# Optimization experiments

Hardware: AMD Instinct MI355X
Metric: run time of the kernel (lower is better)

The kernel has to match this reference:

```python
import jax, jax.numpy as jnp
import numpy as np

NUM_HEADS = 16

def setup_inputs() -> dict:
    key = jax.random.key(0)
    k1, k2, k3 = jax.random.split(key, 3)
    B, N, C = 4, 2048, 1024
    x = jax.random.normal(k1, (B, N, C), dtype=jnp.float32)
    # torch Linear weights are [out_features, in_features]
    w_qkv = jax.random.normal(k2, (3 * C, C), dtype=jnp.float32) * (1.0 / np.sqrt(C))
    w_out = jax.random.normal(k3, (C, C), dtype=jnp.float32) * (1.0 / np.sqrt(C))
    b_out = jnp.zeros((C,), dtype=jnp.float32)
    return {"x": x, "w_qkv": w_qkv, "w_out": w_out, "b_out": b_out}

def reference(x, w_qkv, w_out, b_out):
    B, N, C = x.shape
    H = NUM_HEADS
    D = C // H
    scale = 1.0 / np.sqrt(D).astype(np.float32)
    # qkv projection: [B,N,3C] -> [3,B,H,N,D]
    qkv = (x @ w_qkv.T).reshape(B, N, 3, H, D).transpose(2, 0, 3, 1, 4)
    q, k, v = qkv[0], qkv[1], qkv[2]
    # The torch module's block-wise online softmax telescopes to exact softmax.
    scores = jnp.einsum("bhqd,bhkd->bhqk", q, k) * scale
    attn = jax.nn.softmax(scores, axis=-1)
    out = jnp.einsum("bhqk,bhkd->bhqd", attn, v)  # [B,H,N,D]
    out = out.transpose(0, 2, 1, 3).reshape(B, N, C)
    return out @ w_out.T + b_out
```

## Files before the change

### kernel.cpp

```cpp
#include <hip/hip_runtime.h>

typedef __attribute__((ext_vector_type(8))) short vbf8;
typedef __attribute__((ext_vector_type(4))) float vf4;

#define GLOAD16(g, l) __builtin_amdgcn_global_load_lds( \
    (const __attribute__((address_space(1))) void*)(g),  \
    (__attribute__((address_space(3))) void*)(l), 16, 0, 0)

__device__ __forceinline__ unsigned short f2bf(float f) {
  union { float f; unsigned u; } v; v.f = f;
  return (unsigned short)((v.u + 0x7fffu + ((v.u >> 16) & 1u)) >> 16);
}

__device__ __forceinline__ unsigned short cvt_bf16(float f) {
  __bf16 h = (__bf16)f;
  union { __bf16 h; unsigned short u; } v; v.h = h;
  return v.u;
}

__device__ __forceinline__ vf4 mfma16(vbf8 a, vbf8 b, vf4 c) {
  return __builtin_amdgcn_mfma_f32_16x16x32_bf16(a, b, c, 0, 0, 0);
}

__device__ __forceinline__ int swz(int row, int col) {
  return row * 64 + (col ^ ((row & 7) << 3));
}

__global__ __launch_bounds__(256)
void k_cvt_bf16(const float* __restrict__ in, unsigned short* __restrict__ out, int n4) {
  for (int i = blockIdx.x * blockDim.x + threadIdx.x; i < n4; i += gridDim.x * blockDim.x) {
    float4 v = ((const float4*)in)[i];
    ushort4 o;
    o.x = f2bf(v.x); o.y = f2bf(v.y); o.z = f2bf(v.z); o.w = f2bf(v.w);
    ((ushort4*)out)[i] = o;
  }
}

__global__ __launch_bounds__(256, 2)
void k_gemm_qkv(const unsigned short* __restrict__ A,
                const unsigned short* __restrict__ B,
                unsigned short* __restrict__ qb,
                unsigned short* __restrict__ kb,
                unsigned short* __restrict__ vb) {
  __shared__ unsigned short As[128 * 64];
  __shared__ unsigned short Bs[128 * 64];
  const int tid = threadIdx.x;
  const int lane = tid & 63;
  const int wid = tid >> 6;
  const int wm = wid >> 1, wn = wid & 1;
  const int flat = blockIdx.y * 24 + blockIdx.x;
  const int sw = (flat & 7) * 192 + (flat >> 3);
  const int m0 = (sw / 24) * 128;
  const int n0 = (sw % 24) * 128;
  const int l15 = lane & 15, kg = lane >> 4;
  const int srow = wid * 32 + (lane >> 3);
  const int scol = (lane & 7) * 8;

  vf4 acc[4][4] = {};

  for (int kt = 0; kt < 16; ++kt) {
    __syncthreads();
    const unsigned short* gA = A + (size_t)(m0 + srow) * 1024 + kt * 64 + scol;
    const unsigned short* gB = B + (size_t)(n0 + srow) * 1024 + kt * 64 + scol;
    const unsigned ab = (unsigned)(wid * 32 * 64);
#pragma unroll
    for (int i = 0; i < 4; ++i) {
      GLOAD16(gA + (size_t)i * 8 * 1024, &As[ab + i * 8 * 64]);
      GLOAD16(gB + (size_t)i * 8 * 1024, &Bs[ab + i * 8 * 64]);
    }
    __syncthreads();
#pragma unroll
    for (int kk = 0; kk < 2; ++kk) {
      vbf8 af[4], bfr[4];
#pragma unroll
      for (int mi = 0; mi < 4; ++mi)
        af[mi] = *(const vbf8*)&As[(wm * 64 + mi * 16 + l15) * 64 + kk * 32 + kg * 8];
#pragma unroll
      for (int ni = 0; ni < 4; ++ni)
        bfr[ni] = *(const vbf8*)&Bs[(wn * 64 + ni * 16 + l15) * 64 + kk * 32 + kg * 8];
#pragma unroll
      for (int mi = 0; mi < 4; ++mi)
#pragma unroll
        for (int ni = 0; ni < 4; ++ni)
          acc[mi][ni] = mfma16(af[mi], bfr[ni], acc[mi][ni]);
    }
  }

#pragma unroll
  for (int ni = 0; ni < 4; ++ni) {
    const int c = n0 + wn * 64 + ni * 16 + l15;
    const int which = c >> 10;
    const int hd = c & 1023;
    unsigned short* dst = (which == 0) ? qb : ((which == 1) ? kb : vb);
    const float sc = (which == 0) ? 0.18033688011112042f : 1.0f;
#pragma unroll
    for (int mi = 0; mi < 4; ++mi) {
#pragma unroll
      for (int r = 0; r < 4; ++r) {
        const int m = m0 + wm * 64 + mi * 16 + kg * 4 + r;
        const int b = m >> 11, nn = m & 2047;
        const size_t idx = (((size_t)(b * 16 + (hd >> 6)) * 2048 + nn) * 64) + (hd & 63);
        dst[idx] = f2bf(acc[mi][ni][r] * sc);
      }
    }
  }
}

__global__ __launch_bounds__(256)
void k_transpose_v(const unsigned short* __restrict__ vb, unsigned short* __restrict__ vt) {
  __shared__ unsigned short t[64][72];
  const int bh = blockIdx.y, n0 = blockIdx.x * 64;
  const int tid = threadIdx.x;
#pragma unroll
  for (int p = 0; p < 2; ++p) {
    const int r = p * 32 + (tid >> 3);
    vbf8 v = *(const vbf8*)&vb[((size_t)bh * 2048 + n0 + r) * 64 + (tid & 7) * 8];
    *(vbf8*)&t[r][(tid & 7) * 8] = v;
  }
  __syncthreads();
  const int d = tid >> 2, jb = (tid & 3) * 16;
  unsigned short buf[16];
#pragma unroll
  for (int j = 0; j < 16; ++j) buf[j] = t[jb + j][d];
  unsigned short* o = &vt[((size_t)bh * 64 + d) * 2048 + n0 + jb];
  *(vbf8*)&o[0] = *(vbf8*)&buf[0];
  *(vbf8*)&o[8] = *(vbf8*)&buf[8];
}

__global__ __launch_bounds__(256, 4)
void k_attn(const unsigned short* __restrict__ qb,
            const unsigned short* __restrict__ kb,
            const unsigned short* __restrict__ vt,
            unsigned short* __restrict__ ob) {
  __shared__ unsigned short Ks[2][64 * 64];
  __shared__ unsigned short Vs[64 * 64];
  __shared__ unsigned short Ps[4][32][64];
  const int tid = threadIdx.x, lane = tid & 63, w = tid >> 6;
  const int l15 = lane & 15, kg = lane >> 4;
  const int flat = blockIdx.x;
  const int sw = (flat & 7) * 128 + (flat >> 3);
  const int qt = sw & 15, bh = sw >> 4;

  const unsigned short* Q = qb + ((size_t)bh * 2048 + qt * 128 + w * 32) * 64;
  vbf8 qf[2][2];
#pragma unroll
  for (int qj = 0; qj < 2; ++qj)
#pragma unroll
    for (int kk = 0; kk < 2; ++kk)
      qf[qj][kk] = *(const vbf8*)(Q + (qj * 16 + l15) * 64 + kk * 32 + kg * 8);

  vbf8 onesv;
#pragma unroll
  for (int i = 0; i < 8; ++i) onesv[i] = (short)0x3F80;

  vf4 oacc[2][4] = {};
  vf4 lacc[2] = {};
  float mrun[2] = {-3.0e38f, -3.0e38f};

  const int srow = lane >> 3;
  const int scol = (((lane & 7) ^ srow) * 8);
  const int pswz = (l15 & 7) << 3;
  const unsigned short* gKbase = kb + ((size_t)bh * 2048 + w * 16 + srow) * 64 + scol;
  const unsigned short* gVbase = vt + ((size_t)bh * 64 + w * 16 + srow) * 2048 + scol;

#define STAGE_K(t, b) do { \
    const unsigned short* gK_ = gKbase + (size_t)(t) * 4096; \
    GLOAD16(gK_,       &Ks[b][(w * 16) * 64]); \
    GLOAD16(gK_ + 512, &Ks[b][(w * 16 + 8) * 64]); \
  } while (0)
#define STAGE_V(t) do { \
    const unsigned short* gV_ = gVbase + (size_t)(t) * 64; \
    GLOAD16(gV_,                 &Vs[(w * 16) * 64]); \
    GLOAD16(gV_ + (size_t)16384, &Vs[(w * 16 + 8) * 64]); \
  } while (0)

  STAGE_K(0, 0);
  asm volatile("s_waitcnt vmcnt(0)" ::: "memory");
  __builtin_amdgcn_s_barrier();
  __builtin_amdgcn_sched_barrier(0);

  for (int kt = 0; kt < 32; ++kt) {
    const int cur = kt & 1;
    STAGE_V(kt);
    if (kt + 1 < 32) STAGE_K(kt + 1, cur ^ 1);

    vf4 s[2][4] = {};
    __builtin_amdgcn_s_setprio(1);
#pragma unroll
    for (int kk = 0; kk < 2; ++kk)
#pragma unroll
      for (int ni = 0; ni < 4; ++ni) {
        const vbf8 kf = *(const vbf8*)&Ks[cur][swz(ni * 16 + l15, kk * 32 + kg * 8)];
        s[0][ni] = mfma16(kf, qf[0][kk], s[0][ni]);
        s[1][ni] = mfma16(kf, qf[1][kk], s[1][ni]);
      }
    __builtin_amdgcn_s_setprio(0);

#pragma unroll
    for (int qj = 0; qj < 2; ++qj) {
      float a0 = fmaxf(fmaxf(s[qj][0][0], s[qj][0][1]), fmaxf(s[qj][0][2], s[qj][0][3]));
      float a1 = fmaxf(fmaxf(s[qj][1][0], s[qj][1][1]), fmaxf(s[qj][1][2], s[qj][1][3]));
      float a2 = fmaxf(fmaxf(s[qj][2][0], s[qj][2][1]), fmaxf(s[qj][2][2], s[qj][2][3]));
      float a3 = fmaxf(fmaxf(s[qj][3][0], s[qj][3][1]), fmaxf(s[qj][3][2], s[qj][3][3]));
      float rm = fmaxf(fmaxf(a0, a1), fmaxf(a2, a3));
      rm = fmaxf(rm, __shfl_xor(rm, 16));
      rm = fmaxf(rm, __shfl_xor(rm, 32));

      if (__any(rm > mrun[qj] + 8.0f)) {
        const float mn = fmaxf(mrun[qj], rm);
        const float alpha = __builtin_amdgcn_exp2f(mrun[qj] - mn);
        mrun[qj] = mn;
        float av[4];
#pragma unroll
        for (int r = 0; r < 4; ++r) av[r] = __shfl(alpha, kg * 4 + r);
#pragma unroll
        for (int r = 0; r < 4; ++r) {
          lacc[qj][r] *= av[r];
#pragma unroll
          for (int ni = 0; ni < 4; ++ni) oacc[qj][ni][r] *= av[r];
        }
      }

#pragma unroll
      for (int ni = 0; ni < 4; ++ni) {
        ushort4 pk;
        pk.x = cvt_bf16(__builtin_amdgcn_exp2f(s[qj][ni][0] - mrun[qj]));
        pk.y = cvt_bf16(__builtin_amdgcn_exp2f(s[qj][ni][1] - mrun[qj]));
        pk.z = cvt_bf16(__builtin_amdgcn_exp2f(s[qj][ni][2] - mrun[qj]));
        pk.w = cvt_bf16(__builtin_amdgcn_exp2f(s[qj][ni][3] - mrun[qj]));
        *(ushort4*)&Ps[w][qj * 16 + l15][(ni * 16 + kg * 4) ^ pswz] = pk;
      }
    }

    if (kt + 1 < 32) asm volatile("s_waitcnt vmcnt(2) lgkmcnt(0)" ::: "memory");
    else             asm volatile("s_waitcnt vmcnt(0) lgkmcnt(0)" ::: "memory");
    __builtin_amdgcn_s_barrier();
    __builtin_amdgcn_sched_barrier(0);

    __builtin_amdgcn_s_setprio(1);
#pragma unroll
    for (int kk = 0; kk < 2; ++kk) {
      const vbf8 pf0 = *(const vbf8*)&Ps[w][l15][(kk * 32 + kg * 8) ^ pswz];
      const vbf8 pf1 = *(const vbf8*)&Ps[w][16 + l15][(kk * 32 + kg * 8) ^ pswz];
      lacc[0] = mfma16(pf0, onesv, lacc[0]);
      lacc[1] = mfma16(pf1, onesv, lacc[1]);
#pragma unroll
      for (int ni = 0; ni < 4; ++ni) {
        const vbf8 vf = *(const vbf8*)&Vs[swz(ni * 16 + l15, kk * 32 + kg * 8)];
        oacc[0][ni] = mfma16(pf0, vf, oacc[0][ni]);
        oacc[1][ni] = mfma16(pf1, vf, oacc[1][ni]);
      }
    }
    __builtin_amdgcn_s_setprio(0);

    __syncthreads();
  }
#undef STAGE_K
#undef STAGE_V

  const int b = bh >> 4, h = bh & 15;
#pragma unroll
  for (int qj = 0; qj < 2; ++qj)
#pragma unroll
    for (int r = 0; r < 4; ++r) {
      const float inv = 1.0f / lacc[qj][r];
      const int q = qt * 128 + w * 32 + qj * 16 + kg * 4 + r;
#pragma unroll
      for (int ni = 0; ni < 4; ++ni)
        ob[((size_t)b * 2048 + q) * 1024 + h * 64 + ni * 16 + l15] = cvt_bf16(oacc[qj][ni][r] * inv);
    }
}

__global__ __launch_bounds__(256, 2)
void k_gemm_out(const unsigned short* __restrict__ A,
                const unsigned short* __restrict__ B,
                const float* __restrict__ bias,
                float* __restrict__ out) {
  __shared__ unsigned short As[128 * 64];
  __shared__ unsigned short Bs[128 * 64];
  const int tid = threadIdx.x;
  const int lane = tid & 63;
  const int wid = tid >> 6;
  const int wm = wid >> 1, wn = wid & 1;
  const int flat = blockIdx.y * 8 + blockIdx.x;
  const int sw = (flat & 7) * 64 + (flat >> 3);
  const int m0 = (sw / 8) * 128;
  const int n0 = (sw % 8) * 128;
  const int l15 = lane & 15, kg = lane >> 4;
  const int srow = wid * 32 + (lane >> 3);
  const int scol = (lane & 7) * 8;

  vf4 acc[4][4] = {};

  for (int kt = 0; kt < 16; ++kt) {
    __syncthreads();
    const unsigned short* gA = A + (size_t)(m0 + srow) * 1024 + kt * 64 + scol;
    const unsigned short* gB = B + (size_t)(n0 + srow) * 1024 + kt * 64 + scol;
    const unsigned ab = (unsigned)(wid * 32 * 64);
#pragma unroll
    for (int i = 0; i < 4; ++i) {
      GLOAD16(gA + (size_t)i * 8 * 1024, &As[ab + i * 8 * 64]);
      GLOAD16(gB + (size_t)i * 8 * 1024, &Bs[ab + i * 8 * 64]);
    }
    __syncthreads();
#pragma unroll
    for (int kk = 0; kk < 2; ++kk) {
      vbf8 af[4], bfr[4];
#pragma unroll
      for (int mi = 0; mi < 4; ++mi)
        af[mi] = *(const vbf8*)&As[(wm * 64 + mi * 16 + l15) * 64 + kk * 32 + kg * 8];
#pragma unroll
      for (int ni = 0; ni < 4; ++ni)
        bfr[ni] = *(const vbf8*)&Bs[(wn * 64 + ni * 16 + l15) * 64 + kk * 32 + kg * 8];
#pragma unroll
      for (int mi = 0; mi < 4; ++mi)
#pragma unroll
        for (int ni = 0; ni < 4; ++ni)
          acc[mi][ni] = mfma16(af[mi], bfr[ni], acc[mi][ni]);
    }
  }

#pragma unroll
  for (int ni = 0; ni < 4; ++ni) {
    const int c = n0 + wn * 64 + ni * 16 + l15;
    const float bv = bias[c];
#pragma unroll
    for (int mi = 0; mi < 4; ++mi) {
#pragma unroll
      for (int r = 0; r < 4; ++r) {
        const int m = m0 + wm * 64 + mi * 16 + kg * 4 + r;
        out[(size_t)m * 1024 + c] = acc[mi][ni][r] + bv;
      }
    }
  }
}

extern "C" void kernel_launch(void* const* d_in, const int* in_sizes, int n_in,
                              void* d_out, int out_size, void* d_ws, size_t ws_size,
                              hipStream_t stream) {
  const float* x     = (const float*)d_in[0];
  const float* w_qkv = (const float*)d_in[1];
  const float* w_out = (const float*)d_in[2];
  const float* b_out = (const float*)d_in[3];
  float* out = (float*)d_out;

  char* ws = (char*)d_ws;
  unsigned short* xbf   = (unsigned short*)(ws);
  unsigned short* wqkvb = (unsigned short*)(ws + 16777216);
  unsigned short* woutb = (unsigned short*)(ws + 23068672);
  unsigned short* qbuf  = (unsigned short*)(ws + 25165824);
  unsigned short* kbuf  = (unsigned short*)(ws + 41943040);
  unsigned short* vbuf  = (unsigned short*)(ws + 58720256);
  unsigned short* vtbuf = (unsigned short*)(ws + 75497472);
  unsigned short* aob   = xbf;

  k_cvt_bf16<<<2048, 256, 0, stream>>>(x, xbf, 8388608 / 4);
  k_cvt_bf16<<<768, 256, 0, stream>>>(w_qkv, wqkvb, 3145728 / 4);
  k_cvt_bf16<<<256, 256, 0, stream>>>(w_out, woutb, 1048576 / 4);

  k_gemm_qkv<<<dim3(24, 64), 256, 0, stream>>>(xbf, wqkvb, qbuf, kbuf, vbuf);
  k_transpose_v<<<dim3(32, 64), 256, 0, stream>>>(vbuf, vtbuf);
  k_attn<<<dim3(1024), 256, 0, stream>>>(qbuf, kbuf, vtbuf, aob);
  k_gemm_out<<<dim3(8, 64), 256, 0, stream>>>(aob, woutb, b_out, out);
}
```

Measured before the change: 215.4 us.

## Double-buffer GEMMs with BK=32, fuse V transpose into QKV epilogue

Both GEMMs move from single-buffered BK=64 tiles with two barriers per step to double-buffered BK=32 tiles with XOR-swizzled LDS, prefetching the next tile while MFMAs run. The QKV GEMM becomes a 128x192 tile computed by 512 threads. Its epilogue writes V directly in transposed layout, which removes the separate transpose kernel and its round trip through memory. The attention row-max now uses a chain of three-input max operations. The transposed V stores are strided scalar writes, which may lower store efficiency in the epilogue.

```diff
diff --git a/kernel.cpp b/kernel.cpp
--- a/kernel.cpp
+++ b/kernel.cpp
@@ -20,6 +20,10 @@
 
 __device__ __forceinline__ vf4 mfma16(vbf8 a, vbf8 b, vf4 c) {
   return __builtin_amdgcn_mfma_f32_16x16x32_bf16(a, b, c, 0, 0, 0);
+}
+
+__device__ __forceinline__ float fmax3(float a, float b, float c) {
+  return fmaxf(fmaxf(a, b), c);
 }
 
 __device__ __forceinline__ int swz(int row, int col) {
@@ -36,62 +40,73 @@
   }
 }
 
-__global__ __launch_bounds__(256, 2)
+__global__ __launch_bounds__(512, 4)
 void k_gemm_qkv(const unsigned short* __restrict__ A,
                 const unsigned short* __restrict__ B,
                 unsigned short* __restrict__ qb,
                 unsigned short* __restrict__ kb,
-                unsigned short* __restrict__ vb) {
-  __shared__ unsigned short As[128 * 64];
-  __shared__ unsigned short Bs[128 * 64];
+                unsigned short* __restrict__ vtb) {
+  __shared__ unsigned short As[2][128 * 32];
+  __shared__ unsigned short Bs[2][192 * 32];
   const int tid = threadIdx.x;
   const int lane = tid & 63;
   const int wid = tid >> 6;
-  const int wm = wid >> 1, wn = wid & 1;
-  const int flat = blockIdx.y * 24 + blockIdx.x;
-  const int sw = (flat & 7) * 192 + (flat >> 3);
-  const int m0 = (sw / 24) * 128;
-  const int n0 = (sw % 24) * 128;
+  const int wm = wid >> 2, wn = wid & 3;
   const int l15 = lane & 15, kg = lane >> 4;
-  const int srow = wid * 32 + (lane >> 3);
-  const int scol = (lane & 7) * 8;
-
-  vf4 acc[4][4] = {};
-
-  for (int kt = 0; kt < 16; ++kt) {
+  const int flat = blockIdx.x;
+  const int sw = (flat & 7) * 128 + (flat >> 3);
+  const int m0 = (sw >> 4) * 128;
+  const int n0 = (sw & 15) * 192;
+
+  const int srow = tid >> 2;
+  const int scg = (tid & 3) ^ (srow & 3);
+  const unsigned short* Ag  = A + (size_t)(m0 + srow) * 1024 + scg * 8;
+  const unsigned short* Bg0 = B + (size_t)(n0 + srow) * 1024 + scg * 8;
+  const unsigned short* Bg1 = B + (size_t)(n0 + 128 + srow) * 1024 + scg * 8;
+  const unsigned ldsoff = (unsigned)(wid * 512);
+
+#define STAGE(t, b) do { \
+    const int ko = (t) * 32; \
+    GLOAD16(Ag + ko,  &As[b][ldsoff]); \
+    GLOAD16(Bg0 + ko, &Bs[b][ldsoff]); \
+    if (wid < 4) GLOAD16(Bg1 + ko, &Bs[b][128 * 32 + ldsoff]); \
+  } while (0)
+
+  vf4 acc[4][3] = {};
+  const int rsw = (kg ^ (l15 & 3)) * 8;
+
+  STAGE(0, 0);
+  __syncthreads();
+
+  for (int kt = 0; kt < 32; ++kt) {
+    const int cur = kt & 1;
+    if (kt + 1 < 32) STAGE(kt + 1, cur ^ 1);
+
+    vbf8 af[4], bfr[3];
+#pragma unroll
+    for (int mi = 0; mi < 4; ++mi)
+      af[mi] = *(const vbf8*)&As[cur][(wm * 64 + mi * 16 + l15) * 32 + rsw];
+#pragma unroll
+    for (int ni = 0; ni < 3; ++ni)
+      bfr[ni] = *(const vbf8*)&Bs[cur][(wn * 48 + ni * 16 + l15) * 32 + rsw];
+    __builtin_amdgcn_s_setprio(1);
+#pragma unroll
+    for (int mi = 0; mi < 4; ++mi)
+#pragma unroll
+      for (int ni = 0; ni < 3; ++ni)
+        acc[mi][ni] = mfma16(af[mi], bfr[ni], acc[mi][ni]);
+    __builtin_amdgcn_s_setprio(0);
+
     __syncthreads();
-    const unsigned short* gA = A + (size_t)(m0 + srow) * 1024 + kt * 64 + scol;
-    const unsigned short* gB = B + (size_t)(n0 + srow) * 1024 + kt * 64 + scol;
-    const unsigned ab = (unsigned)(wid * 32 * 64);
-#pragma unroll
-    for (int i = 0; i < 4; ++i) {
-      GLOAD16(gA + (size_t)i * 8 * 1024, &As[ab + i * 8 * 64]);
-      GLOAD16(gB + (size_t)i * 8 * 1024, &Bs[ab + i * 8 * 64]);
-    }
-    __syncthreads();
-#pragma unroll
-    for (int kk = 0; kk < 2; ++kk) {
-      vbf8 af[4], bfr[4];
-#pragma unroll
-      for (int mi = 0; mi < 4; ++mi)
-        af[mi] = *(const vbf8*)&As[(wm * 64 + mi * 16 + l15) * 64 + kk * 32 + kg * 8];
-#pragma unroll
-      for (int ni = 0; ni < 4; ++ni)
-        bfr[ni] = *(const vbf8*)&Bs[(wn * 64 + ni * 16 + l15) * 64 + kk * 32 + kg * 8];
-#pragma unroll
-      for (int mi = 0; mi < 4; ++mi)
-#pragma unroll
-        for (int ni = 0; ni < 4; ++ni)
-          acc[mi][ni] = mfma16(af[mi], bfr[ni], acc[mi][ni]);
-    }
-  }
-
-#pragma unroll
-  for (int ni = 0; ni < 4; ++ni) {
-    const int c = n0 + wn * 64 + ni * 16 + l15;
+  }
+#undef STAGE
+
+#pragma unroll
+  for (int ni = 0; ni < 3; ++ni) {
+    const int c = n0 + wn * 48 + ni * 16 + l15;
     const int which = c >> 10;
     const int hd = c & 1023;
-    unsigned short* dst = (which == 0) ? qb : ((which == 1) ? kb : vb);
+    const int h = hd >> 6, d = hd & 63;
     const float sc = (which == 0) ? 0.18033688011112042f : 1.0f;
 #pragma unroll
     for (int mi = 0; mi < 4; ++mi) {
@@ -99,32 +114,16 @@
       for (int r = 0; r < 4; ++r) {
         const int m = m0 + wm * 64 + mi * 16 + kg * 4 + r;
         const int b = m >> 11, nn = m & 2047;
-        const size_t idx = (((size_t)(b * 16 + (hd >> 6)) * 2048 + nn) * 64) + (hd & 63);
-        dst[idx] = f2bf(acc[mi][ni][r] * sc);
-      }
-    }
-  }
-}
-
-__global__ __launch_bounds__(256)
-void k_transpose_v(const unsigned short* __restrict__ vb, unsigned short* __restrict__ vt) {
-  __shared__ unsigned short t[64][72];
-  const int bh = blockIdx.y, n0 = blockIdx.x * 64;
-  const int tid = threadIdx.x;
-#pragma unroll
-  for (int p = 0; p < 2; ++p) {
-    const int r = p * 32 + (tid >> 3);
-    vbf8 v = *(const vbf8*)&vb[((size_t)bh * 2048 + n0 + r) * 64 + (tid & 7) * 8];
-    *(vbf8*)&t[r][(tid & 7) * 8] = v;
-  }
-  __syncthreads();
-  const int d = tid >> 2, jb = (tid & 3) * 16;
-  unsigned short buf[16];
-#pragma unroll
-  for (int j = 0; j < 16; ++j) buf[j] = t[jb + j][d];
-  unsigned short* o = &vt[((size_t)bh * 64 + d) * 2048 + n0 + jb];
-  *(vbf8*)&o[0] = *(vbf8*)&buf[0];
-  *(vbf8*)&o[8] = *(vbf8*)&buf[8];
+        const unsigned short val = f2bf(acc[mi][ni][r] * sc);
+        if (which == 2) {
+          vtb[((size_t)(b * 16 + h) * 64 + d) * 2048 + nn] = val;
+        } else {
+          unsigned short* dst = (which == 0) ? qb : kb;
+          dst[((size_t)(b * 16 + h) * 2048 + nn) * 64 + d] = val;
+        }
+      }
+    }
+  }
 }
 
 __global__ __launch_bounds__(256, 4)
@@ -198,11 +197,14 @@
 
 #pragma unroll
     for (int qj = 0; qj < 2; ++qj) {
-      float a0 = fmaxf(fmaxf(s[qj][0][0], s[qj][0][1]), fmaxf(s[qj][0][2], s[qj][0][3]));
-      float a1 = fmaxf(fmaxf(s[qj][1][0], s[qj][1][1]), fmaxf(s[qj][1][2], s[qj][1][3]));
-      float a2 = fmaxf(fmaxf(s[qj][2][0], s[qj][2][1]), fmaxf(s[qj][2][2], s[qj][2][3]));
-      float a3 = fmaxf(fmaxf(s[qj][3][0], s[qj][3][1]), fmaxf(s[qj][3][2], s[qj][3][3]));
-      float rm = fmaxf(fmaxf(a0, a1), fmaxf(a2, a3));
+      float rm = fmax3(s[qj][0][0], s[qj][0][1], s[qj][0][2]);
+      rm = fmax3(rm, s[qj][0][3], s[qj][1][0]);
+      rm = fmax3(rm, s[qj][1][1], s[qj][1][2]);
+      rm = fmax3(rm, s[qj][1][3], s[qj][2][0]);
+      rm = fmax3(rm, s[qj][2][1], s[qj][2][2]);
+      rm = fmax3(rm, s[qj][2][3], s[qj][3][0]);
+      rm = fmax3(rm, s[qj][3][1], s[qj][3][2]);
+      rm = fmaxf(rm, s[qj][3][3]);
       rm = fmaxf(rm, __shfl_xor(rm, 16));
       rm = fmaxf(rm, __shfl_xor(rm, 32));
 
@@ -271,54 +273,65 @@
     }
 }
 
-__global__ __launch_bounds__(256, 2)
+__global__ __launch_bounds__(256, 4)
 void k_gemm_out(const unsigned short* __restrict__ A,
                 const unsigned short* __restrict__ B,
                 const float* __restrict__ bias,
                 float* __restrict__ out) {
-  __shared__ unsigned short As[128 * 64];
-  __shared__ unsigned short Bs[128 * 64];
+  __shared__ unsigned short As[2][128 * 32];
+  __shared__ unsigned short Bs[2][128 * 32];
   const int tid = threadIdx.x;
   const int lane = tid & 63;
   const int wid = tid >> 6;
   const int wm = wid >> 1, wn = wid & 1;
+  const int l15 = lane & 15, kg = lane >> 4;
   const int flat = blockIdx.y * 8 + blockIdx.x;
   const int sw = (flat & 7) * 64 + (flat >> 3);
-  const int m0 = (sw / 8) * 128;
-  const int n0 = (sw % 8) * 128;
-  const int l15 = lane & 15, kg = lane >> 4;
-  const int srow = wid * 32 + (lane >> 3);
-  const int scol = (lane & 7) * 8;
+  const int m0 = (sw >> 3) * 128;
+  const int n0 = (sw & 7) * 128;
+
+  const int srow = tid >> 2;
+  const int scg = (tid & 3) ^ (srow & 3);
+  const unsigned short* Ag = A + (size_t)(m0 + srow) * 1024 + scg * 8;
+  const unsigned short* Bg = B + (size_t)(n0 + srow) * 1024 + scg * 8;
+  const unsigned ldsoff = (unsigned)(wid * 512);
+
+#define STAGE(t, b) do { \
+    const int ko = (t) * 32; \
+    GLOAD16(Ag + ko,                     &As[b][ldsoff]); \
+    GLOAD16(Ag + ko + (size_t)64 * 1024, &As[b][64 * 32 + ldsoff]); \
+    GLOAD16(Bg + ko,                     &Bs[b][ldsoff]); \
+    GLOAD16(Bg + ko + (size_t)64 * 1024, &Bs[b][64 * 32 + ldsoff]); \
+  } while (0)
 
   vf4 acc[4][4] = {};
-
-  for (int kt = 0; kt < 16; ++kt) {
+  const int rsw = (kg ^ (l15 & 3)) * 8;
+
+  STAGE(0, 0);
+  __syncthreads();
+
+  for (int kt = 0; kt < 32; ++kt) {
+    const int cur = kt & 1;
+    if (kt + 1 < 32) STAGE(kt + 1, cur ^ 1);
+
+    vbf8 af[4], bfr[4];
+#pragma unroll
+    for (int mi = 0; mi < 4; ++mi)
+      af[mi] = *(const vbf8*)&As[cur][(wm * 64 + mi * 16 + l15) * 32 + rsw];
+#pragma unroll
+    for (int ni = 0; ni < 4; ++ni)
+      bfr[ni] = *(const vbf8*)&Bs[cur][(wn * 64 + ni * 16 + l15) * 32 + rsw];
+    __builtin_amdgcn_s_setprio(1);
+#pragma unroll
+    for (int mi = 0; mi < 4; ++mi)
+#pragma unroll
+      for (int ni = 0; ni < 4; ++ni)
+        acc[mi][ni] = mfma16(af[mi], bfr[ni], acc[mi][ni]);
+    __builtin_amdgcn_s_setprio(0);
+
     __syncthreads();
-    const unsigned short* gA = A + (size_t)(m0 + srow) * 1024 + kt * 64 + scol;
-    const unsigned short* gB = B + (size_t)(n0 + srow) * 1024 + kt * 64 + scol;
-    const unsigned ab = (unsigned)(wid * 32 * 64);
-#pragma unroll
-    for (int i = 0; i < 4; ++i) {
-      GLOAD16(gA + (size_t)i * 8 * 1024, &As[ab + i * 8 * 64]);
-      GLOAD16(gB + (size_t)i * 8 * 1024, &Bs[ab + i * 8 * 64]);
-    }
-    __syncthreads();
-#pragma unroll
-    for (int kk = 0; kk < 2; ++kk) {
-      vbf8 af[4], bfr[4];
-#pragma unroll
-      for (int mi = 0; mi < 4; ++mi)
-        af[mi] = *(const vbf8*)&As[(wm * 64 + mi * 16 + l15) * 64 + kk * 32 + kg * 8];
-#pragma unroll
-      for (int ni = 0; ni < 4; ++ni)
-        bfr[ni] = *(const vbf8*)&Bs[(wn * 64 + ni * 16 + l15) * 64 + kk * 32 + kg * 8];
-#pragma unroll
-      for (int mi = 0; mi < 4; ++mi)
-#pragma unroll
-        for (int ni = 0; ni < 4; ++ni)
-          acc[mi][ni] = mfma16(af[mi], bfr[ni], acc[mi][ni]);
-    }
-  }
+  }
+#undef STAGE
 
 #pragma unroll
   for (int ni = 0; ni < 4; ++ni) {
@@ -350,7 +363,6 @@
   unsigned short* woutb = (unsigned short*)(ws + 23068672);
   unsigned short* qbuf  = (unsigned short*)(ws + 25165824);
   unsigned short* kbuf  = (unsigned short*)(ws + 41943040);
-  unsigned short* vbuf  = (unsigned short*)(ws + 58720256);
   unsigned short* vtbuf = (unsigned short*)(ws + 75497472);
   unsigned short* aob   = xbf;
 
@@ -358,8 +370,7 @@
   k_cvt_bf16<<<768, 256, 0, stream>>>(w_qkv, wqkvb, 3145728 / 4);
   k_cvt_bf16<<<256, 256, 0, stream>>>(w_out, woutb, 1048576 / 4);
 
-  k_gemm_qkv<<<dim3(24, 64), 256, 0, stream>>>(xbf, wqkvb, qbuf, kbuf, vbuf);
-  k_transpose_v<<<dim3(32, 64), 256, 0, stream>>>(vbuf, vtbuf);
+  k_gemm_qkv<<<dim3(1024), 512, 0, stream>>>(xbf, wqkvb, qbuf, kbuf, vtbuf);
   k_attn<<<dim3(1024), 256, 0, stream>>>(qbuf, kbuf, vtbuf, aob);
   k_gemm_out<<<dim3(8, 64), 256, 0, stream>>>(aob, woutb, b_out, out);
 }
```

After: 234.8 us. 9.0% more time.
